# Kernel optimization log

Measured on AMD Instinct MI355X. Metric: run time of the kernel, lower is better.

The kernel has to match this reference:

```python
import jax, jax.numpy as jnp
import numpy as np
import math

B, S, D, H = 4, 1024, 1024, 16
DK = D // H
WINDOW = 128
NEG = -100000.0


def setup_inputs() -> dict:
    key = jax.random.key(0)
    kx, kw1, kb1, kw2, kb2 = jax.random.split(key, 5)
    x = jax.random.normal(kx, (B, S, D), dtype=jnp.float32)
    # sliding-window band mask: True where |i-j| <= WINDOW
    i = jnp.arange(S)
    band = (jnp.abs(i[:, None] - i[None, :]) <= WINDOW)
    mask = jnp.broadcast_to(band, (B, S, S))
    # second structured mask: causal
    causal = (i[:, None] >= i[None, :])
    mask2 = jnp.broadcast_to(causal, (B, S, S))
    scale = 1.0 / math.sqrt(D)
    Wqkv = jax.random.normal(kw1, (D, 3 * D), dtype=jnp.float32) * scale
    bqkv = jax.random.normal(kb1, (3 * D,), dtype=jnp.float32) * 0.01
    Wo = jax.random.normal(kw2, (D, D), dtype=jnp.float32) * scale
    bo = jax.random.normal(kb2, (D,), dtype=jnp.float32) * 0.01
    return {"x": x, "mask": mask, "mask2": mask2, "Wqkv": Wqkv, "bqkv": bqkv, "Wo": Wo, "bo": bo}


def reference(x, mask, mask2, Wqkv, bqkv, Wo, bo):
    b, s, d = x.shape
    qkv = x @ Wqkv + bqkv                      # [b, s, 3d]
    q, k, v = jnp.split(qkv, 3, axis=-1)
    # [b, s, h, dk] -> [b, h, s, dk]
    q = q.reshape(b, s, H, DK).transpose(0, 2, 1, 3)
    k = k.reshape(b, s, H, DK).transpose(0, 2, 1, 3)
    v = v.reshape(b, s, H, DK).transpose(0, 2, 1, 3)
    scores = jnp.einsum('bhtd,bhsd->bhts', q, k) / math.sqrt(DK)
    scores = jnp.where(mask[:, None, :, :], scores, NEG)
    scores = jnp.where(mask2[:, None, :, :], scores, NEG)
    weights = jax.nn.softmax(scores, axis=-1)  # [b, h, t, s]
    context = jnp.einsum('bhts,bhsd->bhtd', weights, v)
    context = context.transpose(0, 2, 1, 3).reshape(b, s, d)
    context = context @ Wo + bo
    return (context, weights)
```

## Files before the change

kernel.cpp:

```cpp
#include <hip/hip_runtime.h>

typedef short bf16x8 __attribute__((ext_vector_type(8)));
typedef float floatx4 __attribute__((ext_vector_type(4)));

__device__ __forceinline__ ushort f2bf(float x) {
  uint u = __float_as_uint(x);
  return (ushort)((u + 0x7fffu + ((u >> 16) & 1u)) >> 16);
}

__global__ __launch_bounds__(256) void k_f32_to_bf16(const float4* __restrict__ in,
                                                     ushort4* __restrict__ out, int n4) {
  int g = blockIdx.x * 256 + threadIdx.x;
  if (g < n4) {
    float4 v = in[g];
    ushort4 o;
    o.x = f2bf(v.x); o.y = f2bf(v.y); o.z = f2bf(v.z); o.w = f2bf(v.w);
    out[g] = o;
  }
}

__global__ __launch_bounds__(256) void k_transpose_bf16(const float* __restrict__ in,
                                                        ushort* __restrict__ out, int K, int N) {
  __shared__ float tile[32][33];
  int n0 = blockIdx.x * 32, k0 = blockIdx.y * 32;
  int tx = threadIdx.x & 31, ty = threadIdx.x >> 5;
  #pragma unroll
  for (int r = ty; r < 32; r += 8)
    tile[r][tx] = in[(size_t)(k0 + r) * N + n0 + tx];
  __syncthreads();
  #pragma unroll
  for (int r = ty; r < 32; r += 8)
    out[(size_t)(n0 + r) * K + k0 + tx] = f2bf(tile[tx][r]);
}

template <int OUT_BF16>
__global__ __launch_bounds__(256) void k_gemm_bt(const ushort* __restrict__ A,
                                                 const ushort* __restrict__ Bt,
                                                 const float* __restrict__ bias,
                                                 void* __restrict__ Cout,
                                                 int M, int N, int K) {
  __shared__ ushort As[128 * 40];
  __shared__ ushort Bs[128 * 40];
  const int t = threadIdx.x;
  const int m0 = blockIdx.y * 128, n0 = blockIdx.x * 128;
  const int w = t >> 6, l = t & 63;
  const int wm = (w & 1) * 64, wn = (w >> 1) * 64;
  const int lr = l & 15, q8 = (l >> 4) * 8;

  const int sr = t >> 2;
  const int sc = (t & 3) * 8;
  const ushort* ga0 = A + (size_t)(m0 + sr) * K + sc;
  const ushort* ga1 = A + (size_t)(m0 + sr + 64) * K + sc;
  const ushort* gb0 = Bt + (size_t)(n0 + sr) * K + sc;
  const ushort* gb1 = Bt + (size_t)(n0 + sr + 64) * K + sc;
  ushort* la0 = As + sr * 40 + sc;
  ushort* la1 = As + (sr + 64) * 40 + sc;
  ushort* lb0 = Bs + sr * 40 + sc;
  ushort* lb1 = Bs + (sr + 64) * 40 + sc;

  floatx4 acc[4][4];
  #pragma unroll
  for (int i = 0; i < 4; ++i)
    #pragma unroll
    for (int j = 0; j < 4; ++j) acc[i][j] = (floatx4){0.f, 0.f, 0.f, 0.f};

  for (int k0 = 0; k0 < K; k0 += 32) {
    uint4 a0 = *(const uint4*)(ga0 + k0);
    uint4 a1 = *(const uint4*)(ga1 + k0);
    uint4 b0 = *(const uint4*)(gb0 + k0);
    uint4 b1 = *(const uint4*)(gb1 + k0);
    __syncthreads();
    *(uint4*)la0 = a0; *(uint4*)la1 = a1;
    *(uint4*)lb0 = b0; *(uint4*)lb1 = b1;
    __syncthreads();
    bf16x8 af[4], bfr[4];
    #pragma unroll
    for (int mi = 0; mi < 4; ++mi)
      af[mi] = *(const bf16x8*)(As + (wm + mi * 16 + lr) * 40 + q8);
    #pragma unroll
    for (int ni = 0; ni < 4; ++ni)
      bfr[ni] = *(const bf16x8*)(Bs + (wn + ni * 16 + lr) * 40 + q8);
    #pragma unroll
    for (int mi = 0; mi < 4; ++mi)
      #pragma unroll
      for (int ni = 0; ni < 4; ++ni)
        acc[mi][ni] = __builtin_amdgcn_mfma_f32_16x16x32_bf16(af[mi], bfr[ni], acc[mi][ni], 0, 0, 0);
  }

  const int rq = (l >> 4) * 4;
  #pragma unroll
  for (int ni = 0; ni < 4; ++ni) {
    int col = n0 + wn + ni * 16 + lr;
    float bv = bias[col];
    #pragma unroll
    for (int mi = 0; mi < 4; ++mi) {
      int row = m0 + wm + mi * 16 + rq;
      #pragma unroll
      for (int r2 = 0; r2 < 4; ++r2) {
        float v = acc[mi][ni][r2] + bv;
        size_t idx = (size_t)(row + r2) * N + col;
        if (OUT_BF16) ((ushort*)Cout)[idx] = f2bf(v);
        else          ((float*)Cout)[idx] = v;
      }
    }
  }
}

__global__ __launch_bounds__(256) void k_attn(const ushort* __restrict__ qkv,
                                              float* __restrict__ wout,
                                              ushort* __restrict__ ctxout) {
  __shared__ float smA[64][68];
  __shared__ float smB[64][68];

  const int t = threadIdx.x;
  const int tj = t & 15, ti = t >> 4;
  const int iblk = blockIdx.x & 15;
  const int h = (blockIdx.x >> 4) & 15;
  const int b = blockIdx.x >> 8;
  const int i0 = iblk * 64;
  const int tok0 = b * 1024 + i0;
  const int qoff = h * 64, koff = 1024 + h * 64, voff = 2048 + h * 64;
  const size_t wbase = ((size_t)(b * 16 + h) * 1024 + i0) * 1024;

  {
    int jstart = i0 - 128; if (jstart < 0) jstart = 0;
    int jend = i0 + 64;
    float4 z = {0.f, 0.f, 0.f, 0.f};
    for (int g = t; g < 64 * 256; g += 256) {
      int r = g >> 8, j = (g & 255) * 4;
      if (j < jstart || j >= jend)
        *(float4*)(wout + wbase + (size_t)r * 1024 + j) = z;
    }
  }

  for (int cc = t; cc < 512; cc += 256) {
    int r = cc >> 3, c8 = (cc & 7) * 8;
    uint4 u = *(const uint4*)(qkv + (size_t)(tok0 + r) * 3072 + qoff + c8);
    float4 f0, f1;
    f0.x = __uint_as_float(u.x << 16); f0.y = __uint_as_float(u.x & 0xffff0000u);
    f0.z = __uint_as_float(u.y << 16); f0.w = __uint_as_float(u.y & 0xffff0000u);
    f1.x = __uint_as_float(u.z << 16); f1.y = __uint_as_float(u.z & 0xffff0000u);
    f1.z = __uint_as_float(u.w << 16); f1.w = __uint_as_float(u.w & 0xffff0000u);
    *(float4*)&smA[r][c8] = f0;
    *(float4*)&smA[r][c8 + 4] = f1;
  }

  float sreg[3][4][4];
  float mrun[4], lrun[4];
  #pragma unroll
  for (int ri = 0; ri < 4; ++ri) { mrun[ri] = -3e38f; lrun[ri] = 0.f; }

  #pragma unroll
  for (int bb = 0; bb < 3; ++bb) {
    const int jb = i0 - 128 + bb * 64;
    if (jb < 0) continue;
    __syncthreads();
    for (int cc = t; cc < 512; cc += 256) {
      int r = cc >> 3, c8 = (cc & 7) * 8;
      uint4 u = *(const uint4*)(qkv + (size_t)(b * 1024 + jb + r) * 3072 + koff + c8);
      float4 f0, f1;
      f0.x = __uint_as_float(u.x << 16); f0.y = __uint_as_float(u.x & 0xffff0000u);
      f0.z = __uint_as_float(u.y << 16); f0.w = __uint_as_float(u.y & 0xffff0000u);
      f1.x = __uint_as_float(u.z << 16); f1.y = __uint_as_float(u.z & 0xffff0000u);
      f1.z = __uint_as_float(u.w << 16); f1.w = __uint_as_float(u.w & 0xffff0000u);
      *(float4*)&smB[r][c8] = f0;
      *(float4*)&smB[r][c8 + 4] = f1;
    }
    __syncthreads();

    float sacc[4][4];
    #pragma unroll
    for (int ri = 0; ri < 4; ++ri)
      #pragma unroll
      for (int ci = 0; ci < 4; ++ci) sacc[ri][ci] = 0.f;

    for (int d4 = 0; d4 < 16; ++d4) {
      float4 qv[4], kv[4];
      #pragma unroll
      for (int ri = 0; ri < 4; ++ri) qv[ri] = *(const float4*)&smA[4 * ti + ri][d4 * 4];
      #pragma unroll
      for (int ci = 0; ci < 4; ++ci) kv[ci] = *(const float4*)&smB[tj + 16 * ci][d4 * 4];
      #pragma unroll
      for (int ri = 0; ri < 4; ++ri)
        #pragma unroll
        for (int ci = 0; ci < 4; ++ci)
          sacc[ri][ci] += qv[ri].x * kv[ci].x + qv[ri].y * kv[ci].y +
                          qv[ri].z * kv[ci].z + qv[ri].w * kv[ci].w;
    }

    #pragma unroll
    for (int ri = 0; ri < 4; ++ri) {
      int gi = i0 + 4 * ti + ri;
      float mx = mrun[ri];
      #pragma unroll
      for (int ci = 0; ci < 4; ++ci) {
        int gj = jb + tj + 16 * ci;
        bool valid = (gj <= gi) && (gi - gj <= 128);
        float s = valid ? sacc[ri][ci] * 0.125f : -3e38f;
        sreg[bb][ri][ci] = s;
        mx = fmaxf(mx, s);
      }
      float sum = lrun[ri] * __expf(mrun[ri] - mx);
      #pragma unroll
      for (int ci = 0; ci < 4; ++ci) {
        float s = sreg[bb][ri][ci];
        sum += (s > -1e37f) ? __expf(s - mx) : 0.f;
      }
      mrun[ri] = mx; lrun[ri] = sum;
    }
  }

  float mfin[4], minv[4];
  #pragma unroll
  for (int ri = 0; ri < 4; ++ri) {
    float m = mrun[ri], lsum = lrun[ri];
    #pragma unroll
    for (int off = 1; off < 16; off <<= 1) {
      float mo = __shfl_xor(m, off, 64);
      float lo = __shfl_xor(lsum, off, 64);
      float mn = fmaxf(m, mo);
      lsum = lsum * __expf(m - mn) + lo * __expf(mo - mn);
      m = mn;
    }
    mfin[ri] = m;
    minv[ri] = 1.0f / lsum;
  }

  float ctx[4][4];
  #pragma unroll
  for (int ri = 0; ri < 4; ++ri)
    #pragma unroll
    for (int ci = 0; ci < 4; ++ci) ctx[ri][ci] = 0.f;

  #pragma unroll
  for (int bb = 0; bb < 3; ++bb) {
    const int jb = i0 - 128 + bb * 64;
    if (jb < 0) continue;
    __syncthreads();
    for (int cc = t; cc < 512; cc += 256) {
      int r = cc >> 3, c8 = (cc & 7) * 8;
      uint4 u = *(const uint4*)(qkv + (size_t)(b * 1024 + jb + r) * 3072 + voff + c8);
      float4 f0, f1;
      f0.x = __uint_as_float(u.x << 16); f0.y = __uint_as_float(u.x & 0xffff0000u);
      f0.z = __uint_as_float(u.y << 16); f0.w = __uint_as_float(u.y & 0xffff0000u);
      f1.x = __uint_as_float(u.z << 16); f1.y = __uint_as_float(u.z & 0xffff0000u);
      f1.z = __uint_as_float(u.w << 16); f1.w = __uint_as_float(u.w & 0xffff0000u);
      *(float4*)&smB[r][c8] = f0;
      *(float4*)&smB[r][c8 + 4] = f1;
    }
    #pragma unroll
    for (int ri = 0; ri < 4; ++ri) {
      int r = 4 * ti + ri;
      float mr = mfin[ri], iv = minv[ri];
      #pragma unroll
      for (int ci = 0; ci < 4; ++ci) {
        float s = sreg[bb][ri][ci];
        float e = (s > -1e37f) ? __expf(s - mr) : 0.f;
        smA[r][tj + 16 * ci] = e;
        wout[wbase + (size_t)r * 1024 + (jb + tj + 16 * ci)] = e * iv;
      }
    }
    __syncthreads();
    #pragma unroll 4
    for (int jl = 0; jl < 64; ++jl) {
      float wv[4], vv[4];
      #pragma unroll
      for (int ri = 0; ri < 4; ++ri) wv[ri] = smA[4 * ti + ri][jl];
      #pragma unroll
      for (int ci = 0; ci < 4; ++ci) vv[ci] = smB[jl][tj + 16 * ci];
      #pragma unroll
      for (int ri = 0; ri < 4; ++ri)
        #pragma unroll
        for (int ci = 0; ci < 4; ++ci) ctx[ri][ci] += wv[ri] * vv[ci];
    }
  }

  #pragma unroll
  for (int ri = 0; ri < 4; ++ri) {
    int r = 4 * ti + ri;
    float iv = minv[ri];
    #pragma unroll
    for (int ci = 0; ci < 4; ++ci)
      ctxout[(size_t)(tok0 + r) * 1024 + qoff + tj + 16 * ci] = f2bf(ctx[ri][ci] * iv);
  }
}

extern "C" void kernel_launch(void* const* d_in, const int* in_sizes, int n_in,
                              void* d_out, int out_size, void* d_ws, size_t ws_size,
                              hipStream_t stream) {
  const float* x    = (const float*)d_in[0];
  const float* Wqkv = (const float*)d_in[3];
  const float* bqkv = (const float*)d_in[4];
  const float* Wo   = (const float*)d_in[5];
  const float* bo   = (const float*)d_in[6];

  float* out_ctx = (float*)d_out;
  float* out_w   = out_ctx + (size_t)4 * 1024 * 1024;

  char* ws = (char*)d_ws;
  ushort* qkv_bf = (ushort*)(ws);
  ushort* ctx_bf = (ushort*)(ws + 25165824);
  ushort* x_bf   = (ushort*)(ws + 33554432);
  ushort* WqkvT  = (ushort*)(ws + 41943040);
  ushort* WoT    = (ushort*)(ws + 48234496);

  k_f32_to_bf16<<<4096, 256, 0, stream>>>((const float4*)x, (ushort4*)x_bf, 1048576);
  k_transpose_bf16<<<dim3(96, 32), 256, 0, stream>>>(Wqkv, WqkvT, 1024, 3072);
  k_transpose_bf16<<<dim3(32, 32), 256, 0, stream>>>(Wo, WoT, 1024, 1024);
  k_gemm_bt<1><<<dim3(24, 32), 256, 0, stream>>>(x_bf, WqkvT, bqkv, qkv_bf, 4096, 3072, 1024);
  k_attn<<<1024, 256, 0, stream>>>(qkv_bf, out_w, ctx_bf);
  k_gemm_bt<0><<<dim3(8, 32), 256, 0, stream>>>(ctx_bf, WoT, bo, out_ctx, 4096, 1024, 1024);
}
```

Before: 450.5 us.

## Use direct global-to-LDS loads in GEMM, vectorize weight stores, narrow output GEMM tile

The GEMM tile loads now go straight from global memory into LDS through global_load_lds, replacing the register staging and the padded LDS rows. The GEMM is templated on the N tile width so the output projection can run with 64-wide tiles and twice as many blocks. In the attention kernel, normalized weight stores are rewritten as coalesced float4 writes read back from shared memory, with per-row inverse sums kept in shared memory. Without the row padding the LDS reads may hit bank conflicts, and the extra LDS pass over the weights adds shared-memory traffic.

New measurement: 448.4 us. No clear change (-0.5%).

```diff
diff --git a/kernel.cpp b/kernel.cpp
--- a/kernel.cpp
+++ b/kernel.cpp
@@ -2,6 +2,13 @@
 
 typedef short bf16x8 __attribute__((ext_vector_type(8)));
 typedef float floatx4 __attribute__((ext_vector_type(4)));
+
+#define GLOBAL_AS __attribute__((address_space(1)))
+#define LDS_AS __attribute__((address_space(3)))
+
+__device__ __forceinline__ void gload_lds16(const ushort* g, ushort* l) {
+  __builtin_amdgcn_global_load_lds((const GLOBAL_AS void*)g, (LDS_AS void*)l, 16, 0, 0);
+}
 
 __device__ __forceinline__ ushort f2bf(float x) {
   uint u = __float_as_uint(x);
@@ -33,63 +40,59 @@
     out[(size_t)(n0 + r) * K + k0 + tx] = f2bf(tile[tx][r]);
 }
 
-template <int OUT_BF16>
+template <int OUT_BF16, int BN>
 __global__ __launch_bounds__(256) void k_gemm_bt(const ushort* __restrict__ A,
                                                  const ushort* __restrict__ Bt,
                                                  const float* __restrict__ bias,
                                                  void* __restrict__ Cout,
                                                  int M, int N, int K) {
-  __shared__ ushort As[128 * 40];
-  __shared__ ushort Bs[128 * 40];
+  constexpr int NI = BN / 32;
+  constexpr int NB = BN / 64;
+  __shared__ ushort As[128 * 32];
+  __shared__ ushort Bs[BN * 32];
   const int t = threadIdx.x;
-  const int m0 = blockIdx.y * 128, n0 = blockIdx.x * 128;
+  const int m0 = blockIdx.y * 128, n0 = blockIdx.x * BN;
   const int w = t >> 6, l = t & 63;
-  const int wm = (w & 1) * 64, wn = (w >> 1) * 64;
+  const int wm = (w & 1) * 64, wn = (w >> 1) * (BN / 2);
   const int lr = l & 15, q8 = (l >> 4) * 8;
-
-  const int sr = t >> 2;
-  const int sc = (t & 3) * 8;
-  const ushort* ga0 = A + (size_t)(m0 + sr) * K + sc;
-  const ushort* ga1 = A + (size_t)(m0 + sr + 64) * K + sc;
-  const ushort* gb0 = Bt + (size_t)(n0 + sr) * K + sc;
-  const ushort* gb1 = Bt + (size_t)(n0 + sr + 64) * K + sc;
-  ushort* la0 = As + sr * 40 + sc;
-  ushort* la1 = As + (sr + 64) * 40 + sc;
-  ushort* lb0 = Bs + sr * 40 + sc;
-  ushort* lb1 = Bs + (sr + 64) * 40 + sc;
-
-  floatx4 acc[4][4];
+  const int lrow = l >> 2, lcol = (l & 3) * 8;
+
+  floatx4 acc[4][NI];
   #pragma unroll
   for (int i = 0; i < 4; ++i)
     #pragma unroll
-    for (int j = 0; j < 4; ++j) acc[i][j] = (floatx4){0.f, 0.f, 0.f, 0.f};
+    for (int j = 0; j < NI; ++j) acc[i][j] = (floatx4){0.f, 0.f, 0.f, 0.f};
 
   for (int k0 = 0; k0 < K; k0 += 32) {
-    uint4 a0 = *(const uint4*)(ga0 + k0);
-    uint4 a1 = *(const uint4*)(ga1 + k0);
-    uint4 b0 = *(const uint4*)(gb0 + k0);
-    uint4 b1 = *(const uint4*)(gb1 + k0);
-    __syncthreads();
-    *(uint4*)la0 = a0; *(uint4*)la1 = a1;
-    *(uint4*)lb0 = b0; *(uint4*)lb1 = b1;
-    __syncthreads();
-    bf16x8 af[4], bfr[4];
+    __syncthreads();
+    #pragma unroll
+    for (int i = 0; i < 2; ++i) {
+      int r0 = (w * 2 + i) * 16;
+      gload_lds16(A + (size_t)(m0 + r0 + lrow) * K + k0 + lcol, As + r0 * 32);
+    }
+    #pragma unroll
+    for (int i = 0; i < NB; ++i) {
+      int r0 = (w * NB + i) * 16;
+      gload_lds16(Bt + (size_t)(n0 + r0 + lrow) * K + k0 + lcol, Bs + r0 * 32);
+    }
+    __syncthreads();
+    bf16x8 af[4], bfr[NI];
     #pragma unroll
     for (int mi = 0; mi < 4; ++mi)
-      af[mi] = *(const bf16x8*)(As + (wm + mi * 16 + lr) * 40 + q8);
-    #pragma unroll
-    for (int ni = 0; ni < 4; ++ni)
-      bfr[ni] = *(const bf16x8*)(Bs + (wn + ni * 16 + lr) * 40 + q8);
+      af[mi] = *(const bf16x8*)(As + (wm + mi * 16 + lr) * 32 + q8);
+    #pragma unroll
+    for (int ni = 0; ni < NI; ++ni)
+      bfr[ni] = *(const bf16x8*)(Bs + (wn + ni * 16 + lr) * 32 + q8);
     #pragma unroll
     for (int mi = 0; mi < 4; ++mi)
       #pragma unroll
-      for (int ni = 0; ni < 4; ++ni)
+      for (int ni = 0; ni < NI; ++ni)
         acc[mi][ni] = __builtin_amdgcn_mfma_f32_16x16x32_bf16(af[mi], bfr[ni], acc[mi][ni], 0, 0, 0);
   }
 
   const int rq = (l >> 4) * 4;
   #pragma unroll
-  for (int ni = 0; ni < 4; ++ni) {
+  for (int ni = 0; ni < NI; ++ni) {
     int col = n0 + wn + ni * 16 + lr;
     float bv = bias[col];
     #pragma unroll
@@ -111,6 +114,7 @@
                                               ushort* __restrict__ ctxout) {
   __shared__ float smA[64][68];
   __shared__ float smB[64][68];
+  __shared__ float smInv[64];
 
   const int t = threadIdx.x;
   const int tj = t & 15, ti = t >> 4;
@@ -225,6 +229,10 @@
     mfin[ri] = m;
     minv[ri] = 1.0f / lsum;
   }
+  if (tj == 0) {
+    #pragma unroll
+    for (int ri = 0; ri < 4; ++ri) smInv[4 * ti + ri] = minv[ri];
+  }
 
   float ctx[4][4];
   #pragma unroll
@@ -251,16 +259,21 @@
     #pragma unroll
     for (int ri = 0; ri < 4; ++ri) {
       int r = 4 * ti + ri;
-      float mr = mfin[ri], iv = minv[ri];
+      float mr = mfin[ri];
       #pragma unroll
       for (int ci = 0; ci < 4; ++ci) {
         float s = sreg[bb][ri][ci];
-        float e = (s > -1e37f) ? __expf(s - mr) : 0.f;
-        smA[r][tj + 16 * ci] = e;
-        wout[wbase + (size_t)r * 1024 + (jb + tj + 16 * ci)] = e * iv;
+        smA[r][tj + 16 * ci] = (s > -1e37f) ? __expf(s - mr) : 0.f;
       }
     }
     __syncthreads();
+    for (int g = t; g < 1024; g += 256) {
+      int r = g >> 4, c = (g & 15) * 4;
+      float4 e4 = *(const float4*)&smA[r][c];
+      float iv = smInv[r];
+      float4 o = {e4.x * iv, e4.y * iv, e4.z * iv, e4.w * iv};
+      *(float4*)(wout + wbase + (size_t)r * 1024 + jb + c) = o;
+    }
     #pragma unroll 4
     for (int jl = 0; jl < 64; ++jl) {
       float wv[4], vv[4];
@@ -307,7 +320,7 @@
   k_f32_to_bf16<<<4096, 256, 0, stream>>>((const float4*)x, (ushort4*)x_bf, 1048576);
   k_transpose_bf16<<<dim3(96, 32), 256, 0, stream>>>(Wqkv, WqkvT, 1024, 3072);
   k_transpose_bf16<<<dim3(32, 32), 256, 0, stream>>>(Wo, WoT, 1024, 1024);
-  k_gemm_bt<1><<<dim3(24, 32), 256, 0, stream>>>(x_bf, WqkvT, bqkv, qkv_bf, 4096, 3072, 1024);
+  k_gemm_bt<1, 128><<<dim3(24, 32), 256, 0, stream>>>(x_bf, WqkvT, bqkv, qkv_bf, 4096, 3072, 1024);
   k_attn<<<1024, 256, 0, stream>>>(qkv_bf, out_w, ctx_bf);
-  k_gemm_bt<0><<<dim3(8, 32), 256, 0, stream>>>(ctx_bf, WoT, bo, out_ctx, 4096, 1024, 1024);
-}
+  k_gemm_bt<0, 64><<<dim3(16, 32), 256, 0, stream>>>(ctx_bf, WoT, bo, out_ctx, 4096, 1024, 1024);
+}
```
